# Kernel optimization log

Hardware: AMD Instinct MI355X
Metric: run time of the kernel (lower is better)

## Reference

```python
import jax, jax.numpy as jnp
import numpy as np
import math

B, S, D, H, DFF = 4, 2048, 1024, 16, 4096
DK = D // H
EPS = 1e-5


def setup_inputs() -> dict:
    key = jax.random.key(0)
    ks = jax.random.split(key, 12)
    sc = 0.02
    inp = {
        "x": jax.random.normal(ks[0], (B, S, D), dtype=jnp.float32),
        "mask": jnp.ones((B, 1, 1, S), dtype=jnp.int32),
        "Wq": jax.random.normal(ks[1], (D, D), jnp.float32) * sc,
        "bq": jnp.zeros((D,), jnp.float32),
        "Wk": jax.random.normal(ks[2], (D, D), jnp.float32) * sc,
        "bk": jnp.zeros((D,), jnp.float32),
        "Wv": jax.random.normal(ks[3], (D, D), jnp.float32) * sc,
        "bv": jnp.zeros((D,), jnp.float32),
        "Wo": jax.random.normal(ks[4], (D, D), jnp.float32) * sc,
        "bo": jnp.zeros((D,), jnp.float32),
        "ln1_g": jnp.ones((D,), jnp.float32),
        "ln1_b": jnp.zeros((D,), jnp.float32),
        "W1": jax.random.normal(ks[5], (D, DFF), jnp.float32) * sc,
        "b1": jnp.zeros((DFF,), jnp.float32),
        "W2": jax.random.normal(ks[6], (DFF, D), jnp.float32) * sc,
        "b2": jnp.zeros((D,), jnp.float32),
        "ln2_g": jnp.ones((D,), jnp.float32),
        "ln2_b": jnp.zeros((D,), jnp.float32),
    }
    return inp


def _layer_norm(x, g, b):
    m = jnp.mean(x, axis=-1, keepdims=True)
    v = jnp.mean(jnp.square(x - m), axis=-1, keepdims=True)
    return (x - m) * jax.lax.rsqrt(v + EPS) * g + b


def reference(x, mask, Wq, bq, Wk, bk, Wv, bv, Wo, bo,
              ln1_g, ln1_b, W1, b1, W2, b2, ln2_g, ln2_b):
    b_, s_, d_ = x.shape
    h_, dk_ = H, DK
    # --- pre-LN attention sublayer ---
    hidden = _layer_norm(x, ln1_g, ln1_b)
    q = (hidden @ Wq + bq).reshape(b_, s_, h_, dk_).transpose(0, 2, 1, 3)  # [B,H,S,dk]
    k = (hidden @ Wk + bk).reshape(b_, s_, h_, dk_).transpose(0, 2, 1, 3)  # [B,H,S,dk]
    # NOTE: original code passes value=key (the value projection is dead code),
    # so K is used both as keys and as values. Reproduced faithfully.
    scores = jnp.einsum("bhqd,bhkd->bhqk", q, k) / math.sqrt(dk_)  # [B,H,S,S]
    scores = jnp.where(mask == 0, jnp.float32(-1e9), scores)
    p_attn = jax.nn.softmax(scores, axis=-1)
    attn_out = jnp.einsum("bhqk,bhkd->bhqd", p_attn, k)  # values == k
    attn_out = attn_out.transpose(0, 2, 1, 3).reshape(b_, s_, d_)
    attn_out = attn_out @ Wo + bo
    x = x + attn_out  # residual (dropout is identity in eval)
    # --- pre-LN FFN sublayer ---
    hidden2 = _layer_norm(x, ln2_g, ln2_b)
    ff = jax.nn.gelu(hidden2 @ W1 + b1, approximate=False) @ W2 + b2
    return x + ff
```

## Files before the change

### kernel.cpp

```cpp
#include <hip/hip_runtime.h>
#include <hip/hip_bf16.h>
#include <math.h>

#define B_   4
#define S_   2048
#define D_   1024
#define H_   16
#define DK_  64
#define DFF_ 4096
#define M_   (B_*S_)

typedef __bf16 bf16;
typedef bf16 bf16x8 __attribute__((ext_vector_type(8)));
typedef bf16 bf16x4 __attribute__((ext_vector_type(4)));
typedef float f32x4 __attribute__((ext_vector_type(4)));

__device__ __forceinline__ void g2lds16(const void* g, void* l) {
  __builtin_amdgcn_global_load_lds(
      (__attribute__((address_space(1))) void*)(void*)g,
      (__attribute__((address_space(3))) void*)l, 16, 0, 0);
}

__device__ __forceinline__ void* swzp(char* base, int row, int byteofs) {
  return base + row * 128 + (byteofs ^ ((row & 7) << 4));
}

__global__ void tcast_all(const float* __restrict__ Wq, const float* __restrict__ Wk,
                          const float* __restrict__ Wo, const float* __restrict__ W1,
                          const float* __restrict__ W2,
                          bf16* __restrict__ WqkT, bf16* __restrict__ WoT,
                          bf16* __restrict__ W1T, bf16* __restrict__ W2T) {
  __shared__ float t[32][33];
  int bid = blockIdx.x;
  const float* src; bf16* dst; int K, N, bx, by;
  if (bid < 1024)      { src = Wq; dst = WqkT;            K = 1024; N = 1024; bx = bid & 31;  by = bid >> 5; }
  else if (bid < 2048) { bid -= 1024; src = Wk; dst = WqkT + 1024 * 1024; K = 1024; N = 1024; bx = bid & 31;  by = bid >> 5; }
  else if (bid < 3072) { bid -= 2048; src = Wo; dst = WoT; K = 1024; N = 1024; bx = bid & 31;  by = bid >> 5; }
  else if (bid < 7168) { bid -= 3072; src = W1; dst = W1T; K = 1024; N = 4096; bx = bid & 127; by = bid >> 7; }
  else                 { bid -= 7168; src = W2; dst = W2T; K = 4096; N = 1024; bx = bid & 31;  by = bid >> 5; }
  int n0 = bx * 32, k0 = by * 32;
  int tx = threadIdx.x, ty = threadIdx.y;
#pragma unroll
  for (int i = 0; i < 4; ++i)
    t[ty + i*8][tx] = src[(size_t)(k0 + ty + i*8) * N + n0 + tx];
  __syncthreads();
#pragma unroll
  for (int i = 0; i < 4; ++i)
    dst[(size_t)(n0 + ty + i*8) * K + k0 + tx] = (bf16)t[tx][ty + i*8];
}

__global__ __launch_bounds__(256)
void ktrans(const bf16* __restrict__ Kt, bf16* __restrict__ KT) {
  __shared__ bf16 t[64][72];
  const int bh = blockIdx.y, s0 = blockIdx.x * 64, tid = threadIdx.x;
  const bf16* src = Kt + (size_t)bh * S_ * DK_;
  bf16* dst = KT + (size_t)bh * DK_ * S_;
#pragma unroll
  for (int i = 0; i < 2; ++i) {
    int c = tid * 2 + i;
    int r = c >> 3, col = (c & 7) * 8;
    *(bf16x8*)&t[r][col] = *(const bf16x8*)&src[(size_t)(s0 + r) * 64 + col];
  }
  __syncthreads();
  const int d = tid >> 2, sc = (tid & 3) * 16;
  bf16x8 v0, v1;
#pragma unroll
  for (int j = 0; j < 8; ++j) { v0[j] = t[sc + j][d]; v1[j] = t[sc + 8 + j][d]; }
  *(bf16x8*)&dst[(size_t)d * S_ + s0 + sc] = v0;
  *(bf16x8*)&dst[(size_t)d * S_ + s0 + sc + 8] = v1;
}

__global__ __launch_bounds__(256)
void ln_fwd(const float* __restrict__ x, const float* __restrict__ g,
            const float* __restrict__ be, bf16* __restrict__ out) {
  int row = blockIdx.x, tid = threadIdx.x;
  const float4 v = *(const float4*)&x[(size_t)row * D_ + tid * 4];
  float s = v.x + v.y + v.z + v.w;
  float q = v.x*v.x + v.y*v.y + v.z*v.z + v.w*v.w;
#pragma unroll
  for (int d = 32; d; d >>= 1) { s += __shfl_down(s, d); q += __shfl_down(q, d); }
  __shared__ float red[8];
  int wave = tid >> 6, lane = tid & 63;
  if (lane == 0) { red[wave*2] = s; red[wave*2+1] = q; }
  __syncthreads();
  float ts = red[0] + red[2] + red[4] + red[6];
  float tq = red[1] + red[3] + red[5] + red[7];
  float mean = ts * (1.0f / D_);
  float var  = tq * (1.0f / D_) - mean * mean;
  float rstd = rsqrtf(var + 1e-5f);
  const float4 gg = *(const float4*)&g[tid * 4];
  const float4 bb = *(const float4*)&be[tid * 4];
  bf16x4 ov;
  ov[0] = (bf16)((v.x - mean) * rstd * gg.x + bb.x);
  ov[1] = (bf16)((v.y - mean) * rstd * gg.y + bb.y);
  ov[2] = (bf16)((v.z - mean) * rstd * gg.z + bb.z);
  ov[3] = (bf16)((v.w - mean) * rstd * gg.w + bb.w);
  *(bf16x4*)&out[(size_t)row * D_ + tid * 4] = ov;
}

template <int EPI>
__global__ __launch_bounds__(256)
void gemm_bt(const bf16* __restrict__ A, const bf16* __restrict__ Bt,
             int M, int N, int K,
             const float* __restrict__ bias, const float* __restrict__ bias2,
             const float* __restrict__ resid, float scale,
             float* __restrict__ outf, bf16* __restrict__ outb,
             bf16* __restrict__ outb2) {
  __shared__ __align__(16) bf16 As[2][128 * 32];
  __shared__ __align__(16) bf16 Bs[2][128 * 32];
  const int tid = threadIdx.x;
  const int wave = tid >> 6, lane = tid & 63;
  const int wr = wave >> 1, wc = wave & 1;

  const int gx = gridDim.x, nwg = gx * gridDim.y;
  int wg = blockIdx.y * gx + blockIdx.x;
  wg = (wg & 7) * (nwg >> 3) + (wg >> 3);
  const long arow = (long)(wg / gx) * 128;
  const long bcol = (long)(wg % gx) * 128;

  f32x4 acc[4][4] = {};

  const int c0 = wave * 2, c1 = wave * 2 + 1;
  const int srow0 = c0 * 16 + (lane >> 2);
  const int srow1 = c1 * 16 + (lane >> 2);
  const int scol = (lane & 3) * 8;
  const int l15 = lane & 15, kof = (lane >> 4) * 8;

  auto stage = [&](int buf, int k0) {
    g2lds16(A  + (arow + srow0) * (long)K + k0 + scol, &As[buf][c0 * 512]);
    g2lds16(A  + (arow + srow1) * (long)K + k0 + scol, &As[buf][c1 * 512]);
    g2lds16(Bt + (bcol + srow0) * (long)K + k0 + scol, &Bs[buf][c0 * 512]);
    g2lds16(Bt + (bcol + srow1) * (long)K + k0 + scol, &Bs[buf][c1 * 512]);
  };

  stage(0, 0);
  __syncthreads();
  int cur = 0;
  for (int k0 = 0; k0 < K; k0 += 32) {
    if (k0 + 32 < K) stage(cur ^ 1, k0 + 32);
    bf16x8 a[4], b[4];
#pragma unroll
    for (int i = 0; i < 4; ++i)
      a[i] = *(const bf16x8*)&As[cur][(wr * 64 + i * 16 + l15) * 32 + kof];
#pragma unroll
    for (int i = 0; i < 4; ++i)
      b[i] = *(const bf16x8*)&Bs[cur][(wc * 64 + i * 16 + l15) * 32 + kof];
#pragma unroll
    for (int mi = 0; mi < 4; ++mi)
#pragma unroll
      for (int ni = 0; ni < 4; ++ni)
        acc[mi][ni] = __builtin_amdgcn_mfma_f32_16x16x32_bf16(
            a[mi], b[ni], acc[mi][ni], 0, 0, 0);
    __syncthreads();
    cur ^= 1;
  }

#pragma unroll
  for (int mi = 0; mi < 4; ++mi) {
#pragma unroll
    for (int ni = 0; ni < 4; ++ni) {
#pragma unroll
      for (int j = 0; j < 4; ++j) {
        long row = arow + wr * 64 + mi * 16 + (lane >> 4) * 4 + j;
        long col = bcol + wc * 64 + ni * 16 + l15;
        float v = acc[mi][ni][j];
        if constexpr (EPI == 0) {
          int bb = (int)(row >> 11), ss = (int)(row & 2047);
          int hh = (int)(col >> 6) & 15, dd = (int)(col & 63);
          size_t idx = (((size_t)(bb * H_ + hh)) * S_ + ss) * DK_ + dd;
          if (col < 1024) outb[idx]  = (bf16)((v + bias[col]) * scale);
          else            outb2[idx] = (bf16)(v + bias2[col - 1024]);
        } else if constexpr (EPI == 1) {
          size_t idx = (size_t)row * N + col;
          outf[idx] = v + bias[col] + resid[idx];
        } else {
          size_t idx = (size_t)row * N + col;
          float t = v + bias[col];
          outb[idx] = (bf16)(0.5f * t * (1.0f + erff(t * 0.70710678118654752f)));
        }
      }
    }
  }
}

__global__ __launch_bounds__(256)
void attn_fwd(const bf16* __restrict__ Q, const bf16* __restrict__ Kk,
              const bf16* __restrict__ KT, const int* __restrict__ mask,
              bf16* __restrict__ O) {
  __shared__ __align__(16) char Kl[2][64 * 128];
  __shared__ __align__(16) char Vl[2][64 * 128];
  __shared__ __align__(16) char Pl[4][16 * 128];

  const int tid = threadIdx.x, wave = tid >> 6, lane = tid & 63;
  const int bh = blockIdx.y, b = bh >> 4, h = bh & 15;
  const int q0 = blockIdx.x * 64;
  const int l15 = lane & 15, q4 = lane >> 4;

  const bf16* Qp = Q  + (size_t)bh * S_ * DK_;
  const bf16* Kp = Kk + (size_t)bh * S_ * DK_;
  const bf16* Tp = KT + (size_t)bh * DK_ * S_;

  const int qrow = q0 + wave * 16 + l15;
  const bf16x8 qf0 = *(const bf16x8*)&Qp[(size_t)qrow * 64 + q4 * 8];
  const bf16x8 qf1 = *(const bf16x8*)&Qp[(size_t)qrow * 64 + 32 + q4 * 8];

  int lz = 0;
  for (int i = tid; i < S_; i += 256) lz |= (mask[b * S_ + i] == 0);
  const bool anyz = __syncthreads_or(lz) != 0;

  const int c0 = tid * 2, c1 = tid * 2 + 1;
  const int sr0 = c0 >> 3, sb0 = c0 & 7;
  const int sr1 = c1 >> 3, sb1 = c1 & 7;

  int poff[16];
#pragma unroll
  for (int nt = 0; nt < 4; ++nt)
#pragma unroll
    for (int j = 0; j < 4; ++j) {
      int r = q4 * 4 + j;
      poff[nt * 4 + j] = r * 128 + ((((nt * 16 + l15) * 2)) ^ ((r & 7) << 4));
    }

  bf16x8 onesv;
#pragma unroll
  for (int i = 0; i < 8; ++i) onesv[i] = (bf16)1.0f;

  f32x4 o[4] = {};
  f32x4 ol = {};
  float m_r[4];
#pragma unroll
  for (int j = 0; j < 4; ++j) m_r[j] = -__builtin_inff();

  bf16x8 a0 = *(const bf16x8*)&Kp[(size_t)sr0 * 64 + sb0 * 8];
  bf16x8 a1 = *(const bf16x8*)&Kp[(size_t)sr1 * 64 + sb1 * 8];
  bf16x8 t0 = *(const bf16x8*)&Tp[(size_t)sr0 * S_ + sb0 * 8];
  bf16x8 t1 = *(const bf16x8*)&Tp[(size_t)sr1 * S_ + sb1 * 8];
  *(bf16x8*)swzp(Kl[0], sr0, sb0 * 16) = a0;
  *(bf16x8*)swzp(Kl[0], sr1, sb1 * 16) = a1;
  *(bf16x8*)swzp(Vl[0], sr0, sb0 * 16) = t0;
  *(bf16x8*)swzp(Vl[0], sr1, sb1 * 16) = t1;
  int cur = 0;

  for (int k0 = 0; k0 < S_; k0 += 64) {
    __syncthreads();

    const int nk = k0 + 64;
    if (nk < S_) {
      a0 = *(const bf16x8*)&Kp[(size_t)(nk + sr0) * 64 + sb0 * 8];
      a1 = *(const bf16x8*)&Kp[(size_t)(nk + sr1) * 64 + sb1 * 8];
      t0 = *(const bf16x8*)&Tp[(size_t)sr0 * S_ + nk + sb0 * 8];
      t1 = *(const bf16x8*)&Tp[(size_t)sr1 * S_ + nk + sb1 * 8];
    }

    f32x4 s[4];
#pragma unroll
    for (int nt = 0; nt < 4; ++nt) {
      bf16x8 kf0 = *(const bf16x8*)swzp(Kl[cur], nt * 16 + l15, q4 * 16);
      bf16x8 kf1 = *(const bf16x8*)swzp(Kl[cur], nt * 16 + l15, 64 + q4 * 16);
      f32x4 z = {};
      z     = __builtin_amdgcn_mfma_f32_16x16x32_bf16(qf0, kf0, z, 0, 0, 0);
      s[nt] = __builtin_amdgcn_mfma_f32_16x16x32_bf16(qf1, kf1, z, 0, 0, 0);
    }
    if (anyz) {
#pragma unroll
      for (int nt = 0; nt < 4; ++nt) {
        int m2 = mask[b * S_ + k0 + nt * 16 + l15];
        if (m2 == 0) {
#pragma unroll
          for (int j = 0; j < 4; ++j) s[nt][j] = -1e9f;
        }
      }
    }

    float tm[4];
#pragma unroll
    for (int j = 0; j < 4; ++j)
      tm[j] = fmaxf(fmaxf(s[0][j], s[1][j]), fmaxf(s[2][j], s[3][j]));
    bool ok = true;
#pragma unroll
    for (int j = 0; j < 4; ++j) ok = ok && (tm[j] <= m_r[j] + 8.0f);
    if (!__all(ok)) {
#pragma unroll
      for (int d = 1; d < 16; d <<= 1)
#pragma unroll
        for (int j = 0; j < 4; ++j)
          tm[j] = fmaxf(tm[j], __shfl_xor(tm[j], d));
#pragma unroll
      for (int j = 0; j < 4; ++j) {
        float mn = fmaxf(m_r[j], tm[j]);
        float sf = __builtin_amdgcn_exp2f(m_r[j] - mn);
        m_r[j] = mn;
        ol[j] *= sf;
#pragma unroll
        for (int nf = 0; nf < 4; ++nf) o[nf][j] *= sf;
      }
    }

#pragma unroll
    for (int nt = 0; nt < 4; ++nt)
#pragma unroll
      for (int j = 0; j < 4; ++j)
        *(bf16*)(&Pl[wave][0] + poff[nt * 4 + j]) =
            (bf16)__builtin_amdgcn_exp2f(s[nt][j] - m_r[j]);

    const bf16x8 pf0 = *(const bf16x8*)swzp(Pl[wave], l15, q4 * 16);
    const bf16x8 pf1 = *(const bf16x8*)swzp(Pl[wave], l15, 64 + q4 * 16);

    ol = __builtin_amdgcn_mfma_f32_16x16x32_bf16(pf0, onesv, ol, 0, 0, 0);
    ol = __builtin_amdgcn_mfma_f32_16x16x32_bf16(pf1, onesv, ol, 0, 0, 0);

#pragma unroll
    for (int nf = 0; nf < 4; ++nf) {
      bf16x8 vf0 = *(const bf16x8*)swzp(Vl[cur], nf * 16 + l15, q4 * 16);
      bf16x8 vf1 = *(const bf16x8*)swzp(Vl[cur], nf * 16 + l15, 64 + q4 * 16);
      o[nf] = __builtin_amdgcn_mfma_f32_16x16x32_bf16(pf0, vf0, o[nf], 0, 0, 0);
      o[nf] = __builtin_amdgcn_mfma_f32_16x16x32_bf16(pf1, vf1, o[nf], 0, 0, 0);
    }

    if (nk < S_) {
      *(bf16x8*)swzp(Kl[cur ^ 1], sr0, sb0 * 16) = a0;
      *(bf16x8*)swzp(Kl[cur ^ 1], sr1, sb1 * 16) = a1;
      *(bf16x8*)swzp(Vl[cur ^ 1], sr0, sb0 * 16) = t0;
      *(bf16x8*)swzp(Vl[cur ^ 1], sr1, sb1 * 16) = t1;
    }
    cur ^= 1;
  }

#pragma unroll
  for (int nf = 0; nf < 4; ++nf)
#pragma unroll
    for (int j = 0; j < 4; ++j) {
      int row = q0 + wave * 16 + q4 * 4 + j;
      int col = h * 64 + nf * 16 + l15;
      O[((size_t)b * S_ + row) * D_ + col] = (bf16)(o[nf][j] / ol[j]);
    }
}

extern "C" void kernel_launch(void* const* d_in, const int* in_sizes, int n_in,
                              void* d_out, int out_size, void* d_ws, size_t ws_size,
                              hipStream_t stream) {
  const float* x    = (const float*)d_in[0];
  const int*   mask = (const int*)d_in[1];
  const float* Wq   = (const float*)d_in[2];
  const float* bq   = (const float*)d_in[3];
  const float* Wk   = (const float*)d_in[4];
  const float* bk   = (const float*)d_in[5];
  const float* Wo   = (const float*)d_in[8];
  const float* bo   = (const float*)d_in[9];
  const float* ln1g = (const float*)d_in[10];
  const float* ln1b = (const float*)d_in[11];
  const float* W1   = (const float*)d_in[12];
  const float* b1   = (const float*)d_in[13];
  const float* W2   = (const float*)d_in[14];
  const float* b2   = (const float*)d_in[15];
  const float* ln2g = (const float*)d_in[16];
  const float* ln2b = (const float*)d_in[17];
  float* out = (float*)d_out;

  char* w = (char*)d_ws;
  auto alloc = [&](size_t bytes) {
    void* p = (void*)w;
    w += (bytes + 255) & ~(size_t)255;
    return p;
  };
  bf16* xln  = (bf16*)alloc((size_t)M_ * D_ * 2);
  bf16* WqkT = (bf16*)alloc((size_t)2 * D_ * D_ * 2);
  bf16* WoT  = (bf16*)alloc((size_t)D_ * D_ * 2);
  bf16* W1T  = (bf16*)alloc((size_t)D_ * DFF_ * 2);
  bf16* W2T  = (bf16*)alloc((size_t)D_ * DFF_ * 2);
  bf16* Qt   = (bf16*)alloc((size_t)M_ * D_ * 2);
  bf16* Kt   = (bf16*)alloc((size_t)M_ * D_ * 2);
  bf16* KTt  = (bf16*)alloc((size_t)M_ * D_ * 2);
  bf16* attn = (bf16*)alloc((size_t)M_ * D_ * 2);
  float* x2  = (float*)alloc((size_t)M_ * D_ * 4);
  bf16* h2   = (bf16*)alloc((size_t)M_ * D_ * 2);
  bf16* act  = (bf16*)alloc((size_t)M_ * DFF_ * 2);

  tcast_all<<<11264, dim3(32, 8), 0, stream>>>(Wq, Wk, Wo, W1, W2,
                                               WqkT, WoT, W1T, W2T);

  ln_fwd<<<M_, 256, 0, stream>>>(x, ln1g, ln1b, xln);

  gemm_bt<0><<<dim3(16, 64), 256, 0, stream>>>(
      xln, WqkT, M_, 2048, 1024, bq, bk, nullptr,
      0.125f * 1.4426950408889634f, nullptr, Qt, Kt);

  ktrans<<<dim3(S_ / 64, B_ * H_), 256, 0, stream>>>(Kt, KTt);

  attn_fwd<<<dim3(S_ / 64, B_ * H_), 256, 0, stream>>>(Qt, Kt, KTt, mask, attn);

  gemm_bt<1><<<dim3(8, 64), 256, 0, stream>>>(attn, WoT, M_, 1024, 1024,
                                              bo, nullptr, x, 1.0f,
                                              x2, nullptr, nullptr);

  ln_fwd<<<M_, 256, 0, stream>>>(x2, ln2g, ln2b, h2);

  gemm_bt<2><<<dim3(32, 64), 256, 0, stream>>>(h2, W1T, M_, 4096, 1024,
                                               b1, nullptr, nullptr, 1.0f,
                                               nullptr, act, nullptr);
  gemm_bt<1><<<dim3(8, 64), 256, 0, stream>>>(act, W2T, M_, 1024, 4096,
                                              b2, nullptr, x2, 1.0f,
                                              out, nullptr, nullptr);
}
```

Baseline: 597.7 us.

## Replace GEMM with 256x256-tile 8-wave kernel using ping-pong LDS pipeline

```diff
diff --git a/kernel.cpp b/kernel.cpp
--- a/kernel.cpp
+++ b/kernel.cpp
@@ -24,6 +24,13 @@
 __device__ __forceinline__ void* swzp(char* base, int row, int byteofs) {
   return base + row * 128 + (byteofs ^ ((row & 7) << 4));
 }
+
+#define FENCE_ asm volatile("" ::: "memory")
+#define BARR_  do { FENCE_; __builtin_amdgcn_s_barrier(); FENCE_; } while (0)
+#define VMW4_  asm volatile("s_waitcnt vmcnt(4)" ::: "memory")
+#define VMW0_  asm volatile("s_waitcnt vmcnt(0)" ::: "memory")
+#define LGW_   do { asm volatile("s_waitcnt lgkmcnt(0)" ::: "memory"); \
+                    __builtin_amdgcn_sched_barrier(0); } while (0)
 
 __global__ void tcast_all(const float* __restrict__ Wq, const float* __restrict__ Wk,
                           const float* __restrict__ Wo, const float* __restrict__ W1,
@@ -98,70 +105,120 @@
   *(bf16x4*)&out[(size_t)row * D_ + tid * 4] = ov;
 }
 
-template <int EPI>
-__global__ __launch_bounds__(256)
-void gemm_bt(const bf16* __restrict__ A, const bf16* __restrict__ Bt,
-             int M, int N, int K,
-             const float* __restrict__ bias, const float* __restrict__ bias2,
-             const float* __restrict__ resid, float scale,
-             float* __restrict__ outf, bf16* __restrict__ outb,
-             bf16* __restrict__ outb2) {
-  __shared__ __align__(16) bf16 As[2][128 * 32];
-  __shared__ __align__(16) bf16 Bs[2][128 * 32];
-  const int tid = threadIdx.x;
-  const int wave = tid >> 6, lane = tid & 63;
-  const int wr = wave >> 1, wc = wave & 1;
+template <int EPI, int KK>
+__global__ __launch_bounds__(512, 2)
+void gemm8p(const bf16* __restrict__ A, const bf16* __restrict__ Bt, int N,
+            const float* __restrict__ bias, const float* __restrict__ bias2,
+            const float* __restrict__ resid, float scale,
+            float* __restrict__ outf, bf16* __restrict__ outb,
+            bf16* __restrict__ outb2) {
+  constexpr int NT = KK / 64;
+  __shared__ __align__(16) bf16 Ab[2][256 * 64];
+  __shared__ __align__(16) bf16 Bb[2][256 * 64];
+  const int tid = threadIdx.x, wave = tid >> 6, lane = tid & 63;
+  const int wr = wave >> 2, wc = wave & 3;
+  const int l15 = lane & 15, q4 = lane >> 4;
 
   const int gx = gridDim.x, nwg = gx * gridDim.y;
   int wg = blockIdx.y * gx + blockIdx.x;
   wg = (wg & 7) * (nwg >> 3) + (wg >> 3);
-  const long arow = (long)(wg / gx) * 128;
-  const long bcol = (long)(wg % gx) * 128;
-
-  f32x4 acc[4][4] = {};
-
-  const int c0 = wave * 2, c1 = wave * 2 + 1;
-  const int srow0 = c0 * 16 + (lane >> 2);
-  const int srow1 = c1 * 16 + (lane >> 2);
-  const int scol = (lane & 3) * 8;
-  const int l15 = lane & 15, kof = (lane >> 4) * 8;
-
-  auto stage = [&](int buf, int k0) {
-    g2lds16(A  + (arow + srow0) * (long)K + k0 + scol, &As[buf][c0 * 512]);
-    g2lds16(A  + (arow + srow1) * (long)K + k0 + scol, &As[buf][c1 * 512]);
-    g2lds16(Bt + (bcol + srow0) * (long)K + k0 + scol, &Bs[buf][c0 * 512]);
-    g2lds16(Bt + (bcol + srow1) * (long)K + k0 + scol, &Bs[buf][c1 * 512]);
-  };
-
-  stage(0, 0);
-  __syncthreads();
-  int cur = 0;
-  for (int k0 = 0; k0 < K; k0 += 32) {
-    if (k0 + 32 < K) stage(cur ^ 1, k0 + 32);
-    bf16x8 a[4], b[4];
-#pragma unroll
-    for (int i = 0; i < 4; ++i)
-      a[i] = *(const bf16x8*)&As[cur][(wr * 64 + i * 16 + l15) * 32 + kof];
-#pragma unroll
-    for (int i = 0; i < 4; ++i)
-      b[i] = *(const bf16x8*)&Bs[cur][(wc * 64 + i * 16 + l15) * 32 + kof];
-#pragma unroll
-    for (int mi = 0; mi < 4; ++mi)
-#pragma unroll
-      for (int ni = 0; ni < 4; ++ni)
-        acc[mi][ni] = __builtin_amdgcn_mfma_f32_16x16x32_bf16(
-            a[mi], b[ni], acc[mi][ni], 0, 0, 0);
-    __syncthreads();
-    cur ^= 1;
+  const long arow = (long)(wg / gx) * 256;
+  const long bcol = (long)(wg % gx) * 256;
+
+  const int srow  = lane >> 3;
+  const int sslot = (lane & 7) ^ srow;
+  const bf16* gA = A  + (size_t)(arow + wave * 16 + srow) * KK + sslot * 8;
+  const bf16* gB = Bt + (size_t)(bcol + wave * 16 + srow) * KK + sslot * 8;
+
+  char* const ab0 = (char*)&Ab[0][0];
+  char* const ab1 = (char*)&Ab[1][0];
+  char* const bb0 = (char*)&Bb[0][0];
+  char* const bb1 = (char*)&Bb[1][0];
+  const int aoff0 = (wr * 128 + l15) * 128;
+  const int boff0 = (wc * 64 + l15) * 128;
+  const int sw    = (l15 & 7) << 4;
+  const int kq0   = (q4 * 16) ^ sw;
+  const int kq1   = (64 + q4 * 16) ^ sw;
+
+  f32x4 acc[8][4] = {};
+  bf16x8 af[4][2], bq[4][2];
+
+#define STG(dst, gsrc, half, kt) do {                                        \
+    long kc_ = (long)(((kt) < NT) ? (kt) : (NT - 1)) * 64;                   \
+    g2lds16((gsrc) + (long)((half) * 128) * KK + kc_,                        \
+            &(dst)[((half) * 128 + wave * 16) * 64]);                        \
+    g2lds16((gsrc) + (long)((half) * 128 + 8) * KK + kc_,                    \
+            &(dst)[((half) * 128 + wave * 16 + 8) * 64]);                    \
+  } while (0)
+
+#define RDA(base, half) do {                                                 \
+    _Pragma("unroll")                                                        \
+    for (int m_ = 0; m_ < 4; ++m_) {                                         \
+      af[m_][0] = *(const bf16x8*)((base) + aoff0 + ((half)*4+m_)*2048 + kq0);\
+      af[m_][1] = *(const bf16x8*)((base) + aoff0 + ((half)*4+m_)*2048 + kq1);\
+    } } while (0)
+
+#define RDB(base, nh) do {                                                   \
+    _Pragma("unroll")                                                        \
+    for (int n_ = 0; n_ < 2; ++n_) {                                         \
+      bq[(nh)*2+n_][0] = *(const bf16x8*)((base) + boff0 + ((nh)*2+n_)*2048 + kq0);\
+      bq[(nh)*2+n_][1] = *(const bf16x8*)((base) + boff0 + ((nh)*2+n_)*2048 + kq1);\
+    } } while (0)
+
+#define QUAD(mh, nh) do {                                                    \
+    __builtin_amdgcn_s_setprio(1);                                          \
+    _Pragma("unroll")                                                        \
+    for (int ks_ = 0; ks_ < 2; ++ks_)                                        \
+      _Pragma("unroll")                                                      \
+      for (int m_ = 0; m_ < 4; ++m_)                                         \
+        _Pragma("unroll")                                                    \
+        for (int n_ = 0; n_ < 2; ++n_)                                       \
+          acc[(mh)*4+m_][(nh)*2+n_] = __builtin_amdgcn_mfma_f32_16x16x32_bf16(\
+              af[m_][ks_], bq[(nh)*2+n_][ks_], acc[(mh)*4+m_][(nh)*2+n_],    \
+              0, 0, 0);                                                      \
+    __builtin_amdgcn_s_setprio(0);                                          \
+  } while (0)
+
+  STG(Bb[0], gB, 0, 0); STG(Bb[0], gB, 1, 0);
+  STG(Ab[0], gA, 0, 0); STG(Ab[0], gA, 1, 0);
+  STG(Bb[1], gB, 0, 1); STG(Bb[1], gB, 1, 1);
+
+  for (int it = 0; it < NT / 2; ++it) {
+    const int t = it * 2;
+    VMW4_; BARR_;
+    RDA(ab0, 0); RDB(bb0, 0);
+    STG(Ab[1], gA, 0, t + 1);
+    LGW_; QUAD(0, 0); BARR_;
+    RDB(bb0, 1);
+    STG(Ab[1], gA, 1, t + 1);
+    LGW_; QUAD(0, 1); BARR_;
+    RDA(ab0, 1);
+    STG(Bb[0], gB, 0, t + 2);
+    LGW_; QUAD(1, 0); BARR_;
+    STG(Bb[0], gB, 1, t + 2);
+    QUAD(1, 1); BARR_;
+    VMW4_; BARR_;
+    RDA(ab1, 0); RDB(bb1, 0);
+    STG(Ab[0], gA, 0, t + 2);
+    LGW_; QUAD(0, 0); BARR_;
+    RDB(bb1, 1);
+    STG(Ab[0], gA, 1, t + 2);
+    LGW_; QUAD(0, 1); BARR_;
+    RDA(ab1, 1);
+    STG(Bb[1], gB, 0, t + 3);
+    LGW_; QUAD(1, 0); BARR_;
+    STG(Bb[1], gB, 1, t + 3);
+    QUAD(1, 1); BARR_;
   }
-
-#pragma unroll
-  for (int mi = 0; mi < 4; ++mi) {
+  VMW0_;
+
+#pragma unroll
+  for (int mi = 0; mi < 8; ++mi) {
 #pragma unroll
     for (int ni = 0; ni < 4; ++ni) {
 #pragma unroll
       for (int j = 0; j < 4; ++j) {
-        long row = arow + wr * 64 + mi * 16 + (lane >> 4) * 4 + j;
+        long row = arow + wr * 128 + mi * 16 + q4 * 4 + j;
         long col = bcol + wc * 64 + ni * 16 + l15;
         float v = acc[mi][ni][j];
         if constexpr (EPI == 0) {
@@ -175,12 +232,16 @@
           outf[idx] = v + bias[col] + resid[idx];
         } else {
           size_t idx = (size_t)row * N + col;
-          float t = v + bias[col];
-          outb[idx] = (bf16)(0.5f * t * (1.0f + erff(t * 0.70710678118654752f)));
+          float tt = v + bias[col];
+          outb[idx] = (bf16)(0.5f * tt * (1.0f + erff(tt * 0.70710678118654752f)));
         }
       }
     }
   }
+#undef STG
+#undef RDA
+#undef RDB
+#undef QUAD
 }
 
 __global__ __launch_bounds__(256)
@@ -381,24 +442,22 @@
 
   ln_fwd<<<M_, 256, 0, stream>>>(x, ln1g, ln1b, xln);
 
-  gemm_bt<0><<<dim3(16, 64), 256, 0, stream>>>(
-      xln, WqkT, M_, 2048, 1024, bq, bk, nullptr,
+  gemm8p<0, 1024><<<dim3(8, 32), 512, 0, stream>>>(
+      xln, WqkT, 2048, bq, bk, nullptr,
       0.125f * 1.4426950408889634f, nullptr, Qt, Kt);
 
   ktrans<<<dim3(S_ / 64, B_ * H_), 256, 0, stream>>>(Kt, KTt);
 
   attn_fwd<<<dim3(S_ / 64, B_ * H_), 256, 0, stream>>>(Qt, Kt, KTt, mask, attn);
 
-  gemm_bt<1><<<dim3(8, 64), 256, 0, stream>>>(attn, WoT, M_, 1024, 1024,
-                                              bo, nullptr, x, 1.0f,
-                                              x2, nullptr, nullptr);
+  gemm8p<1, 1024><<<dim3(4, 32), 512, 0, stream>>>(
+      attn, WoT, 1024, bo, nullptr, x, 1.0f, x2, nullptr, nullptr);
 
   ln_fwd<<<M_, 256, 0, stream>>>(x2, ln2g, ln2b, h2);
 
-  gemm_bt<2><<<dim3(32, 64), 256, 0, stream>>>(h2, W1T, M_, 4096, 1024,
-                                               b1, nullptr, nullptr, 1.0f,
-                                               nullptr, act, nullptr);
-  gemm_bt<1><<<dim3(8, 64), 256, 0, stream>>>(act, W2T, M_, 1024, 4096,
-                                              b2, nullptr, x2, 1.0f,
-                                              out, nullptr, nullptr);
-}
+  gemm8p<2, 1024><<<dim3(16, 32), 512, 0, stream>>>(
+      h2, W1T, 4096, b1, nullptr, nullptr, 1.0f, nullptr, act, nullptr);
+
+  gemm8p<1, 4096><<<dim3(4, 32), 512, 0, stream>>>(
+      act, W2T, 1024, b2, nullptr, x2, 1.0f, out, nullptr, nullptr);
+}
```

New measurement: 604.5 us. Within noise of the previous version (+1.1%).
